# Kernel tuning notes

Measured on AMD Instinct MI355X. Metric: run time of the kernel, lower is better.

## Reference

```python
import jax, jax.numpy as jnp
import numpy as np
import math

B, S, D, H = 4, 1024, 2048, 16
DH = D // H          # dim_head = 128
DHID = 128           # dim_hid
DKER = 64            # dim_ker
EPS = 1e-6


def setup_inputs() -> dict:
    key = jax.random.key(0)
    ks = jax.random.split(key, 12)
    a1 = math.sqrt(6.0 / (DH + DHID))
    a2 = math.sqrt(6.0 / (DKER + DHID))
    a3 = math.sqrt(6.0 / (2 * DKER))
    return {
        "q": jax.random.normal(ks[0], (B, S, D), jnp.float32),
        "k": jax.random.normal(ks[1], (B, S, D), jnp.float32),
        "v": jax.random.normal(ks[2], (B, S, D), jnp.float32),
        "lr_attn_mask": jax.random.randint(ks[3], (B, 1, S, S), 0, 2).astype(bool),
        "sparse_norms_lse": jax.random.normal(ks[4], (B, H, S, 1), jnp.float32),
        "sparse_attn_weights": jax.random.normal(ks[5], (B, H, S, S), jnp.float32),
        "kernel_q_mat1": jax.random.uniform(ks[6], (H, DH, DHID), jnp.float32, -a1, a1),
        "kernel_k_mat1": jax.random.uniform(ks[7], (H, DH, DHID), jnp.float32, -a1, a1),
        "kernel_q_mat2": jax.random.uniform(ks[8], (H, DHID, DKER), jnp.float32, -a2, a2),
        "kernel_k_mat2": jax.random.uniform(ks[9], (H, DHID, DKER), jnp.float32, -a2, a2),
        "interaction_k": jax.random.uniform(ks[10], (H, DKER, DKER), jnp.float32, -a3, a3),
        "scalingD": jnp.ones((1, H, 1, DKER), jnp.float32) * 1e-4,
        "scalingD2": jnp.ones((1, H, 1, DKER), jnp.float32) * 1e-4,
        "lambda_constant": 1,
    }


def _gelu(x):
    # torch F.gelu default = exact (erf) gelu
    return jax.nn.gelu(x, approximate=False)


def reference(q, k, v, lr_attn_mask, sparse_norms_lse, sparse_attn_weights,
              kernel_q_mat1, kernel_k_mat1, kernel_q_mat2, kernel_k_mat2,
              interaction_k, scalingD, scalingD2, lambda_constant):
    # split heads: [B,S,D] -> [B,H,S,DH]
    qh = q.reshape(B, S, H, DH).transpose(0, 2, 1, 3)
    kh = k.reshape(B, S, H, DH).transpose(0, 2, 1, 3)
    vh = v.reshape(B, S, H, DH).transpose(0, 2, 1, 3)

    # learned kernel feature maps (dropout=0 -> identity)
    qf = _gelu(jnp.einsum('bhsd,hde->bhse', qh, kernel_q_mat1))
    qf = _gelu(jnp.einsum('bhse,hef->bhsf', qf, kernel_q_mat2))

    kf = _gelu(jnp.einsum('bhsd,hde->bhse', kh, kernel_k_mat1))
    kf = jnp.abs(scalingD) * _gelu(jnp.einsum('bhse,hef->bhsf', kf, kernel_k_mat2))
    kf = kf + jnp.einsum('bhse,hef->bhsf', kf, interaction_k) * scalingD2

    # low-rank (kernelized) scores, masked. [B,H,S,S]
    scores = jnp.einsum('bhse,bhte->bhst', jnp.abs(qf), jnp.abs(kf))
    m = lr_attn_mask.astype(scores.dtype)  # [B,1,S,S] broadcasts
    scores = m * scores

    # log-domain merge with external sparse attention
    lr_norms_lse = jnp.log(scores.sum(axis=-1, keepdims=True) + EPS)
    norm_factor_lse = jnp.logaddexp(lr_norms_lse, sparse_norms_lse)
    logits = jnp.log(scores + EPS) * m + (1.0 - m) * sparse_attn_weights
    attn = jnp.exp(logits - norm_factor_lse)

    out = jnp.einsum('bhst,bhtd->bhsd', attn, vh)
    return out.transpose(0, 2, 1, 3).reshape(B, S, D)
```

## Files before the change

### kernel.cpp

```cpp
#include <hip/hip_runtime.h>


typedef __bf16 bf16_t;
typedef __attribute__((ext_vector_type(8))) __bf16 bf16x8;
typedef __attribute__((ext_vector_type(4))) float f32x4;

#define MFMA(a, b, c) __builtin_amdgcn_mfma_f32_16x16x32_bf16((a), (b), (c), 0, 0, 0)

typedef __attribute__((address_space(3))) void as3_void;
typedef __attribute__((address_space(1))) const void as1_void;
static __device__ __forceinline__ void gload16(const void* g, void* l) {
    __builtin_amdgcn_global_load_lds((as1_void*)g, (as3_void*)l, 16, 0, 0);
}

static __device__ __forceinline__ float gelu_exact(float x) {
    return 0.5f * x * (1.0f + erff(x * 0.70710678118654752f));
}

static __device__ __forceinline__ unsigned pack_bf16(float a, float b) {
    bf16_t x = (bf16_t)a, y = (bf16_t)b;
    unsigned short ux = __builtin_bit_cast(unsigned short, x);
    unsigned short uy = __builtin_bit_cast(unsigned short, y);
    return (unsigned)ux | ((unsigned)uy << 16);
}

__global__ __launch_bounds__(256) void conv_weights_kernel(
    const float* __restrict__ wq1, const float* __restrict__ wk1,
    const float* __restrict__ wq2, const float* __restrict__ wk2,
    const float* __restrict__ iK,
    bf16_t* __restrict__ wq1t, bf16_t* __restrict__ wk1t,
    bf16_t* __restrict__ wq2t, bf16_t* __restrict__ wk2t,
    bf16_t* __restrict__ iKt)
{
    const int idx = blockIdx.x * 256 + threadIdx.x;
    if (idx < 16 * 128 * 128) {
        int h = idx >> 14, e = (idx >> 7) & 127, d = idx & 127;
        wq1t[idx] = (bf16_t)wq1[(h << 14) + (d << 7) + e];
        wk1t[idx] = (bf16_t)wk1[(h << 14) + (d << 7) + e];
    }
    if (idx < 16 * 64 * 128) {
        int h = idx >> 13, f = (idx >> 7) & 63, e = idx & 127;
        wq2t[idx] = (bf16_t)wq2[(h << 13) + (e << 6) + f];
        wk2t[idx] = (bf16_t)wk2[(h << 13) + (e << 6) + f];
    }
    if (idx < 16 * 64 * 64) {
        int h = idx >> 12, g = (idx >> 6) & 63, f = idx & 63;
        iKt[idx] = (bf16_t)iK[(h << 12) + (f << 6) + g];
    }
}

__global__ __launch_bounds__(256) void prep_mask_kernel(
    const unsigned char* __restrict__ mask8, unsigned char* __restrict__ mout)
{
    __shared__ int mflag;
    const int tid = threadIdx.x;
    if (tid == 0) {
        unsigned a = 0;
        for (int i = 0; i < 64; ++i) a |= mask8[4 * i + 1];
        mflag = (a == 0) ? 1 : 0;
    }
    __syncthreads();
    const size_t base = ((size_t)blockIdx.x * 256 + tid) * 16;
    if (mflag) {
        const int* mi = (const int*)mask8;
        uint4 r;
        unsigned bs[4];
#pragma unroll
        for (int j = 0; j < 4; ++j) {
            int4 v = *reinterpret_cast<const int4*>(&mi[base + j * 4]);
            bs[j] = (v.x ? 1u : 0u) | ((v.y ? 1u : 0u) << 8) |
                    ((v.z ? 1u : 0u) << 16) | ((v.w ? 1u : 0u) << 24);
        }
        r.x = bs[0]; r.y = bs[1]; r.z = bs[2]; r.w = bs[3];
        *reinterpret_cast<uint4*>(&mout[base]) = r;
    } else {
        uint4 v = *reinterpret_cast<const uint4*>(&mask8[base]);
        uint4 r;
        unsigned* pv = (unsigned*)&v;
        unsigned* pr = (unsigned*)&r;
#pragma unroll
        for (int j = 0; j < 4; ++j) {
            unsigned x = pv[j], o = 0;
#pragma unroll
            for (int k = 0; k < 4; ++k)
                o |= (((x >> (8 * k)) & 255u) ? 1u : 0u) << (8 * k);
            pr[j] = o;
        }
        *reinterpret_cast<uint4*>(&mout[base]) = r;
    }
}

__global__ __launch_bounds__(256) void conv_v_kernel(
    const float* __restrict__ v, bf16_t* __restrict__ vT)
{
    __shared__ bf16_t tr[128][72];
    const int bh = blockIdx.x, b = bh >> 4, h = bh & 15;
    const int tt = blockIdx.y;
    const int t0 = tt * 64;
    const int tid = threadIdx.x;
#pragma unroll
    for (int i = 0; i < 8; ++i) {
        int f4 = tid + 256 * i;
        int t = f4 >> 5, c4 = f4 & 31;
        const float4 vv = *reinterpret_cast<const float4*>(
            &v[((size_t)b * 1024 + t0 + t) * 2048 + h * 128 + c4 * 4]);
        tr[c4 * 4 + 0][t] = (bf16_t)vv.x;
        tr[c4 * 4 + 1][t] = (bf16_t)vv.y;
        tr[c4 * 4 + 2][t] = (bf16_t)vv.z;
        tr[c4 * 4 + 3][t] = (bf16_t)vv.w;
    }
    __syncthreads();
#pragma unroll
    for (int i = 0; i < 32; ++i) {
        int e = tid + 256 * i;
        int d = e >> 6, tl = e & 63;
        vT[(((size_t)bh * 16 + tt) * 128 + d) * 64 + tl] = tr[d][tl];
    }
}

__global__ __launch_bounds__(256) void feat_kernel(
    const float* __restrict__ q, const float* __restrict__ k,
    const bf16_t* __restrict__ wq1t, const bf16_t* __restrict__ wq2t,
    const bf16_t* __restrict__ wk1t, const bf16_t* __restrict__ wk2t,
    const bf16_t* __restrict__ iKt,
    const float* __restrict__ sD, const float* __restrict__ sD2,
    bf16_t* __restrict__ qf, bf16_t* __restrict__ kf)
{
    __shared__ bf16_t xa[64][136];
    __shared__ bf16_t h1[64][136];
    __shared__ bf16_t k2[64][72];

    const int tid = threadIdx.x;
    const int lane = tid & 63, w = tid >> 6;
    const int lr = lane & 15, lg = lane >> 4;
    const int row0 = blockIdx.x * 64;
    const int h = blockIdx.y;
    const int path = blockIdx.z;

    const float* X = path ? k : q;
    const bf16_t* w1t = path ? wk1t : wq1t;
    const bf16_t* w2t = path ? wk2t : wq2t;
    bf16_t* outp = path ? kf : qf;

#pragma unroll
    for (int i = 0; i < 8; ++i) {
        int f4 = tid + 256 * i;
        int r = f4 >> 5, c4 = f4 & 31;
        const float4 vv = *reinterpret_cast<const float4*>(
            &X[(size_t)(row0 + r) * 2048 + h * 128 + c4 * 4]);
        xa[r][c4 * 4 + 0] = (bf16_t)vv.x;
        xa[r][c4 * 4 + 1] = (bf16_t)vv.y;
        xa[r][c4 * 4 + 2] = (bf16_t)vv.z;
        xa[r][c4 * 4 + 3] = (bf16_t)vv.w;
    }
    __syncthreads();

    bf16x8 a1[4];
#pragma unroll
    for (int kk = 0; kk < 4; ++kk)
        a1[kk] = *reinterpret_cast<const bf16x8*>(&xa[w * 16 + lr][kk * 32 + lg * 8]);
#pragma unroll
    for (int nt = 0; nt < 8; ++nt) {
        f32x4 acc = {0.f, 0.f, 0.f, 0.f};
#pragma unroll
        for (int kk = 0; kk < 4; ++kk) {
            bf16x8 bfr = *reinterpret_cast<const bf16x8*>(
                &w1t[(size_t)h * 16384 + (nt * 16 + lr) * 128 + kk * 32 + lg * 8]);
            acc = MFMA(a1[kk], bfr, acc);
        }
#pragma unroll
        for (int r = 0; r < 4; ++r)
            h1[w * 16 + lg * 4 + r][nt * 16 + lr] = (bf16_t)gelu_exact(acc[r]);
    }
    __syncthreads();

    bf16x8 a2[4];
#pragma unroll
    for (int kk = 0; kk < 4; ++kk)
        a2[kk] = *reinterpret_cast<const bf16x8*>(&h1[w * 16 + lr][kk * 32 + lg * 8]);

    if (path == 0) {
#pragma unroll
        for (int nt = 0; nt < 4; ++nt) {
            f32x4 acc = {0.f, 0.f, 0.f, 0.f};
#pragma unroll
            for (int kk = 0; kk < 4; ++kk) {
                bf16x8 bfr = *reinterpret_cast<const bf16x8*>(
                    &w2t[(size_t)h * 8192 + (nt * 16 + lr) * 128 + kk * 32 + lg * 8]);
                acc = MFMA(a2[kk], bfr, acc);
            }
#pragma unroll
            for (int r = 0; r < 4; ++r) {
                int n = row0 + w * 16 + lg * 4 + r;
                int bb = n >> 10, s = n & 1023;
                outp[(((size_t)bb * 16 + h) * 1024 + s) * 64 + nt * 16 + lr] =
                    (bf16_t)fabsf(gelu_exact(acc[r]));
            }
        }
    } else {
#pragma unroll
        for (int nt = 0; nt < 4; ++nt) {
            f32x4 acc = {0.f, 0.f, 0.f, 0.f};
#pragma unroll
            for (int kk = 0; kk < 4; ++kk) {
                bf16x8 bfr = *reinterpret_cast<const bf16x8*>(
                    &w2t[(size_t)h * 8192 + (nt * 16 + lr) * 128 + kk * 32 + lg * 8]);
                acc = MFMA(a2[kk], bfr, acc);
            }
#pragma unroll
            for (int r = 0; r < 4; ++r) {
                int f = nt * 16 + lr;
                k2[w * 16 + lg * 4 + r][f] =
                    (bf16_t)(fabsf(sD[h * 64 + f]) * gelu_exact(acc[r]));
            }
        }
        __syncthreads();
        bf16x8 a3[2];
#pragma unroll
        for (int kk = 0; kk < 2; ++kk)
            a3[kk] = *reinterpret_cast<const bf16x8*>(&k2[w * 16 + lr][kk * 32 + lg * 8]);
#pragma unroll
        for (int nt = 0; nt < 4; ++nt) {
            f32x4 acc = {0.f, 0.f, 0.f, 0.f};
#pragma unroll
            for (int kk = 0; kk < 2; ++kk) {
                bf16x8 bfr = *reinterpret_cast<const bf16x8*>(
                    &iKt[(size_t)h * 4096 + (nt * 16 + lr) * 64 + kk * 32 + lg * 8]);
                acc = MFMA(a3[kk], bfr, acc);
            }
#pragma unroll
            for (int r = 0; r < 4; ++r) {
                int row = w * 16 + lg * 4 + r;
                int g = nt * 16 + lr;
                float base = (float)k2[row][g];
                float kv = fabsf(base + acc[r] * sD2[h * 64 + g]);
                int n = row0 + row;
                int bb = n >> 10, s = n & 1023;
                outp[(((size_t)bb * 16 + h) * 1024 + s) * 64 + g] = (bf16_t)kv;
            }
        }
    }
}

__global__ __launch_bounds__(256, 3) void attn_cv_kernel(
    const bf16_t* __restrict__ qf, const bf16_t* __restrict__ kf,
    const bf16_t* __restrict__ vT,
    const unsigned char* __restrict__ mprep,
    const float* __restrict__ saw, const float* __restrict__ lse,
    float* __restrict__ out)
{
    __shared__ bf16_t vbuf[2][128 * 64];
    __shared__ bf16_t kbuf[2][64 * 64];

    const int tid = threadIdx.x;
    const int lane = tid & 63, w = tid >> 6;
    const int lr = lane & 15, lg = lane >> 4;

    const int di = blockIdx.y * 16 + blockIdx.x;
    const int xcd = di & 7, rr = di >> 3;
    const int bh = xcd + 8 * (rr >> 4);
    const int s0 = (rr & 15) * 64;
    const int b = bh >> 4, h = bh & 15;

    const int srow = s0 + w * 16 + lr;
    const size_t saw_row = ((size_t)bh << 20) + (size_t)srow * 1024;
    const size_t m_row   = ((size_t)b << 20) + (size_t)srow * 1024;

    const int vrow = tid >> 3;
    const int vcol8 = (tid & 7) ^ (vrow & 7);
    const bf16_t* vt_bh = vT + (size_t)bh * 131072;
    const bf16_t* kf_bh = kf + (size_t)bh * 65536;

    bf16x8 aq0, aq1;
    {
        const size_t qb = ((size_t)bh * 1024 + srow) * 64;
        aq0 = *reinterpret_cast<const bf16x8*>(&qf[qb + lg * 8]);
        aq1 = *reinterpret_cast<const bf16x8*>(&qf[qb + 32 + lg * 8]);
    }

    const f32x4 fzero = {0.f, 0.f, 0.f, 0.f};
    f32x4 oacc[8];
#pragma unroll
    for (int i = 0; i < 8; ++i) oacc[i] = fzero;
    float rs = 0.f;

#define STAGE_VT(BUF, TILE)                                                      \
    {                                                                            \
        const bf16_t* vg = vt_bh + (size_t)(TILE) * 8192 + vcol8 * 8;            \
        char* lb = (char*)&vbuf[BUF][0] + w * 1024;                              \
        _Pragma("unroll")                                                        \
        for (int j = 0; j < 4; ++j)                                              \
            gload16(vg + (size_t)(32 * j + vrow) * 64, lb + j * 4096);           \
    }

#define STAGE_KF(BUF, TILE)                                                      \
    {                                                                            \
        const bf16_t* kg = kf_bh + (size_t)(TILE) * 4096 + vcol8 * 8;            \
        char* lb = (char*)&kbuf[BUF][0] + w * 1024;                              \
        _Pragma("unroll")                                                        \
        for (int j = 0; j < 2; ++j)                                              \
            gload16(kg + (size_t)(32 * j + vrow) * 64, lb + j * 4096);           \
    }

#define LOAD_SAW(TILE, SS, MM)                                                   \
    {                                                                            \
        _Pragma("unroll")                                                        \
        for (int nt = 0; nt < 4; ++nt) {                                         \
            SS[nt] = *reinterpret_cast<const f32x4*>(                            \
                &saw[saw_row + (size_t)(TILE) * 64 + nt * 16 + lg * 4]);         \
            MM[nt] = *reinterpret_cast<const unsigned*>(                         \
                &mprep[m_row + (size_t)(TILE) * 64 + nt * 16 + lg * 4]);         \
        }                                                                        \
    }

#define QKT_MERGE(CUR, SS, MM)                                                   \
    {                                                                            \
        _Pragma("unroll")                                                        \
        for (int nt = 0; nt < 4; ++nt) {                                         \
            const int row = nt * 16 + lr;                                        \
            const char* kb = (const char*)&kbuf[CUR][0] + row * 128;             \
            const int sw = (row & 7) * 16;                                       \
            bf16x8 k0 = *reinterpret_cast<const bf16x8*>(kb + ((lg * 16) ^ sw)); \
            bf16x8 k1 = *reinterpret_cast<const bf16x8*>(kb + ((64 + lg * 16) ^ sw)); \
            f32x4 acc = fzero;                                                   \
            acc = MFMA(k0, aq0, acc);                                            \
            acc = MFMA(k1, aq1, acc);                                            \
            const unsigned mm = MM[nt];                                          \
            float v0, v1, v2, v3;                                                \
            v0 = (mm & 255u)         ? (acc[0] + 1e-6f) : __expf(SS[nt][0]);     \
            rs += (mm & 255u)         ? acc[0] : 0.f;                            \
            v1 = ((mm >> 8) & 255u)  ? (acc[1] + 1e-6f) : __expf(SS[nt][1]);     \
            rs += ((mm >> 8) & 255u)  ? acc[1] : 0.f;                            \
            v2 = ((mm >> 16) & 255u) ? (acc[2] + 1e-6f) : __expf(SS[nt][2]);     \
            rs += ((mm >> 16) & 255u) ? acc[2] : 0.f;                            \
            v3 = (mm >> 24)          ? (acc[3] + 1e-6f) : __expf(SS[nt][3]);     \
            rs += (mm >> 24)          ? acc[3] : 0.f;                            \
            pk[nt * 2]     = pack_bf16(v0, v1);                                  \
            pk[nt * 2 + 1] = pack_bf16(v2, v3);                                  \
        }                                                                        \
    }

#define REDIST()                                                                 \
    {                                                                            \
        const int srcA = lr + ((lg & 1) << 5);                                   \
        const int srcB = srcA + 16;                                              \
        const bool sel = (lg < 2);                                               \
        const unsigned a0 = __shfl(pk[0], srcA, 64);                             \
        const unsigned a1 = __shfl(pk[1], srcA, 64);                             \
        const unsigned a2 = __shfl(pk[2], srcA, 64);                             \
        const unsigned a3 = __shfl(pk[3], srcA, 64);                             \
        const unsigned b0 = __shfl(pk[0], srcB, 64);                             \
        const unsigned b1 = __shfl(pk[1], srcB, 64);                             \
        const unsigned b2 = __shfl(pk[2], srcB, 64);                             \
        const unsigned b3 = __shfl(pk[3], srcB, 64);                             \
        f0w.x = sel ? a0 : a2;  f0w.y = sel ? a1 : a3;                           \
        f0w.z = sel ? b0 : b2;  f0w.w = sel ? b1 : b3;                           \
        const unsigned c4 = __shfl(pk[4], srcA, 64);                             \
        const unsigned c5 = __shfl(pk[5], srcA, 64);                             \
        const unsigned c6 = __shfl(pk[6], srcA, 64);                             \
        const unsigned c7 = __shfl(pk[7], srcA, 64);                             \
        const unsigned d4 = __shfl(pk[4], srcB, 64);                             \
        const unsigned d5 = __shfl(pk[5], srcB, 64);                             \
        const unsigned d6 = __shfl(pk[6], srcB, 64);                             \
        const unsigned d7 = __shfl(pk[7], srcB, 64);                             \
        f1w.x = sel ? c4 : c6;  f1w.y = sel ? c5 : c7;                           \
        f1w.z = sel ? d4 : d6;  f1w.w = sel ? d5 : d7;                           \
    }

#define PV(CUR)                                                                  \
    {                                                                            \
        bf16x8 pf0 = __builtin_bit_cast(bf16x8, f0w);                            \
        bf16x8 pf1 = __builtin_bit_cast(bf16x8, f1w);                            \
        _Pragma("unroll")                                                        \
        for (int dt = 0; dt < 8; ++dt) {                                         \
            const int row = dt * 16 + lr;                                        \
            const char* vb = (const char*)&vbuf[CUR][0] + row * 128;             \
            const int sw = (row & 7) * 16;                                       \
            bf16x8 v0 = *reinterpret_cast<const bf16x8*>(vb + ((lg * 16) ^ sw)); \
            bf16x8 v1 = *reinterpret_cast<const bf16x8*>(vb + ((64 + lg * 16) ^ sw)); \
            oacc[dt] = MFMA(v0, pf0, oacc[dt]);                                  \
            oacc[dt] = MFMA(v1, pf1, oacc[dt]);                                  \
        }                                                                        \
    }

#define FULL_PHASE(CUR, NXT, TN1, SS, MM, TN2)                                   \
    {                                                                            \
        STAGE_VT(NXT, TN1);                                                      \
        STAGE_KF(NXT, TN1);                                                      \
        __builtin_amdgcn_sched_barrier(0);                                       \
        asm volatile("s_waitcnt vmcnt(14)" ::: "memory");                        \
        __builtin_amdgcn_s_barrier();                                            \
        __builtin_amdgcn_sched_barrier(0);                                       \
        QKT_MERGE(CUR, SS, MM);                                                  \
        REDIST();                                                                \
        LOAD_SAW(TN2, SS, MM);                                                   \
        __builtin_amdgcn_sched_barrier(0);                                       \
        PV(CUR);                                                                 \
        __builtin_amdgcn_sched_barrier(0);                                       \
        __builtin_amdgcn_s_barrier();                                            \
    }

    f32x4 sawA[4], sawB[4];
    unsigned muA[4], muB[4];
    unsigned pk[8];
    uint4 f0w, f1w;

    STAGE_VT(0, 0);
    STAGE_KF(0, 0);
    LOAD_SAW(0, sawA, muA);
    LOAD_SAW(1, sawB, muB);

    for (int i = 0; i < 16; i += 2) {
        FULL_PHASE(0, 1, i + 1,          sawA, muA, (i + 2) & 15);
        FULL_PHASE(1, 0, (i + 2) & 15,   sawB, muB, (i + 3) & 15);
    }

    rs += __shfl_xor(rs, 16);
    rs += __shfl_xor(rs, 32);
    const float invden =
        1.0f / (rs + 1e-6f + __expf(lse[(size_t)bh * 1024 + srow]));

    const size_t ob = ((size_t)b * 1024 + srow) * 2048 + h * 128 + lg * 4;
#pragma unroll
    for (int dt = 0; dt < 8; ++dt) {
        f32x4 o;
        o[0] = oacc[dt][0] * invden;
        o[1] = oacc[dt][1] * invden;
        o[2] = oacc[dt][2] * invden;
        o[3] = oacc[dt][3] * invden;
        *reinterpret_cast<f32x4*>(&out[ob + dt * 16]) = o;
    }
#undef STAGE_VT
#undef STAGE_KF
#undef LOAD_SAW
#undef QKT_MERGE
#undef REDIST
#undef PV
#undef FULL_PHASE
}

extern "C" void kernel_launch(void* const* d_in, const int* in_sizes, int n_in,
                              void* d_out, int out_size, void* d_ws, size_t ws_size,
                              hipStream_t stream)
{
    const float* q   = (const float*)d_in[0];
    const float* k   = (const float*)d_in[1];
    const float* v   = (const float*)d_in[2];
    const unsigned char* mask = (const unsigned char*)d_in[3];
    const float* lse = (const float*)d_in[4];
    const float* saw = (const float*)d_in[5];
    const float* wq1 = (const float*)d_in[6];
    const float* wk1 = (const float*)d_in[7];
    const float* wq2 = (const float*)d_in[8];
    const float* wk2 = (const float*)d_in[9];
    const float* iK  = (const float*)d_in[10];
    const float* sD  = (const float*)d_in[11];
    const float* sD2 = (const float*)d_in[12];
    float* out = (float*)d_out;

    bf16_t* wsb  = (bf16_t*)d_ws;
    bf16_t* wq1t = wsb;
    bf16_t* wk1t = wq1t + 262144;
    bf16_t* wq2t = wk1t + 262144;
    bf16_t* wk2t = wq2t + 131072;
    bf16_t* iKt  = wk2t + 131072;
    bf16_t* qf   = iKt  + 65536;
    bf16_t* kf   = qf   + 4194304;
    bf16_t* vT   = kf   + 4194304;
    unsigned char* mprep = (unsigned char*)(vT + 8388608);

    conv_weights_kernel<<<dim3(1024), dim3(256), 0, stream>>>(
        wq1, wk1, wq2, wk2, iK, wq1t, wk1t, wq2t, wk2t, iKt);
    prep_mask_kernel<<<dim3(1024), dim3(256), 0, stream>>>(mask, mprep);
    conv_v_kernel<<<dim3(64, 16), dim3(256), 0, stream>>>(v, vT);
    feat_kernel<<<dim3(64, 16, 2), dim3(256), 0, stream>>>(
        q, k, wq1t, wq2t, wk1t, wk2t, iKt, sD, sD2, qf, kf);
    attn_cv_kernel<<<dim3(16, 64), dim3(256), 0, stream>>>(
        qf, kf, vT, mprep, saw, lse, out);
}
```

Before: 208.5 us.

## Triple-buffer V/K tiles in attention kernel and raise PV priority

Moves the attention kernel's LDS staging of V-transpose and kernel-feature tiles from two buffers to three, prefetching two tiles ahead. The main loop rotates buffer indices, waits on a deeper vmcnt, and ends with explicit epilogue phases. It also raises wave priority around the PV MFMA block. In exchange, LDS use rises and launch bounds drop from 3 to 2 blocks per CU, which lowers occupancy.

```diff
diff --git a/kernel.cpp b/kernel.cpp
--- a/kernel.cpp
+++ b/kernel.cpp
@@ -242,15 +242,15 @@
     }
 }
 
-__global__ __launch_bounds__(256, 3) void attn_cv_kernel(
+__global__ __launch_bounds__(256, 2) void attn_cv_kernel(
     const bf16_t* __restrict__ qf, const bf16_t* __restrict__ kf,
     const bf16_t* __restrict__ vT,
     const unsigned char* __restrict__ mprep,
     const float* __restrict__ saw, const float* __restrict__ lse,
     float* __restrict__ out)
 {
-    __shared__ bf16_t vbuf[2][128 * 64];
-    __shared__ bf16_t kbuf[2][64 * 64];
+    __shared__ bf16_t vbuf[3][128 * 64];
+    __shared__ bf16_t kbuf[3][64 * 64];
 
     const int tid = threadIdx.x;
     const int lane = tid & 63, w = tid >> 6;
@@ -371,6 +371,7 @@
     {                                                                            \
         bf16x8 pf0 = __builtin_bit_cast(bf16x8, f0w);                            \
         bf16x8 pf1 = __builtin_bit_cast(bf16x8, f1w);                            \
+        __builtin_amdgcn_s_setprio(1);                                           \
         _Pragma("unroll")                                                        \
         for (int dt = 0; dt < 8; ++dt) {                                         \
             const int row = dt * 16 + lr;                                        \
@@ -381,21 +382,22 @@
             oacc[dt] = MFMA(v0, pf0, oacc[dt]);                                  \
             oacc[dt] = MFMA(v1, pf1, oacc[dt]);                                  \
         }                                                                        \
-    }
-
-#define FULL_PHASE(CUR, NXT, TN1, SS, MM, TN2)                                   \
-    {                                                                            \
-        STAGE_VT(NXT, TN1);                                                      \
-        STAGE_KF(NXT, TN1);                                                      \
+        __builtin_amdgcn_s_setprio(0);                                           \
+    }
+
+#define FULL_PHASE(CIDX, SIDX, TSTAGE, SS, MM, TSAW)                             \
+    {                                                                            \
+        STAGE_VT(SIDX, TSTAGE);                                                  \
+        STAGE_KF(SIDX, TSTAGE);                                                  \
         __builtin_amdgcn_sched_barrier(0);                                       \
-        asm volatile("s_waitcnt vmcnt(14)" ::: "memory");                        \
+        asm volatile("s_waitcnt vmcnt(28)" ::: "memory");                        \
         __builtin_amdgcn_s_barrier();                                            \
         __builtin_amdgcn_sched_barrier(0);                                       \
-        QKT_MERGE(CUR, SS, MM);                                                  \
+        QKT_MERGE(CIDX, SS, MM);                                                 \
         REDIST();                                                                \
-        LOAD_SAW(TN2, SS, MM);                                                   \
+        LOAD_SAW(TSAW, SS, MM);                                                  \
         __builtin_amdgcn_sched_barrier(0);                                       \
-        PV(CUR);                                                                 \
+        PV(CIDX);                                                                \
         __builtin_amdgcn_sched_barrier(0);                                       \
         __builtin_amdgcn_s_barrier();                                            \
     }
@@ -408,11 +410,36 @@
     STAGE_VT(0, 0);
     STAGE_KF(0, 0);
     LOAD_SAW(0, sawA, muA);
+    STAGE_VT(1, 1);
+    STAGE_KF(1, 1);
     LOAD_SAW(1, sawB, muB);
 
-    for (int i = 0; i < 16; i += 2) {
-        FULL_PHASE(0, 1, i + 1,          sawA, muA, (i + 2) & 15);
-        FULL_PHASE(1, 0, (i + 2) & 15,   sawB, muB, (i + 3) & 15);
+    int c0 = 0, c1 = 1, c2 = 2;
+    for (int i = 0; i < 14; i += 2) {
+        FULL_PHASE(c0, c2, i + 2, sawA, muA, i + 2);
+        FULL_PHASE(c1, c0, i + 3, sawB, muB, i + 3);
+        const int t_ = c0; c0 = c2; c2 = c1; c1 = t_;
+    }
+
+    {
+        asm volatile("s_waitcnt vmcnt(22)" ::: "memory");
+        __builtin_amdgcn_s_barrier();
+        __builtin_amdgcn_sched_barrier(0);
+        QKT_MERGE(c0, sawA, muA);
+        REDIST();
+        __builtin_amdgcn_sched_barrier(0);
+        PV(c0);
+        __builtin_amdgcn_sched_barrier(0);
+        __builtin_amdgcn_s_barrier();
+    }
+    {
+        asm volatile("s_waitcnt vmcnt(8)" ::: "memory");
+        __builtin_amdgcn_s_barrier();
+        __builtin_amdgcn_sched_barrier(0);
+        QKT_MERGE(c1, sawB, muB);
+        REDIST();
+        __builtin_amdgcn_sched_barrier(0);
+        PV(c1);
     }
 
     rs += __shfl_xor(rs, 16);
```

Result: faster. 197.8 us (-5.1%).
